# Performance work log

Hardware: AMD Instinct MI355X
Metric: run time of the kernel (lower is better)

The kernel has to match this reference:

```python
import jax, jax.numpy as jnp
import numpy as np

B, N, D, E, MULT = 4, 512, 1024, 8, 4
H = D * MULT
CAPACITY_FACTOR = 1.0
EPSILON = 1e-6


def setup_inputs() -> dict:
    key = jax.random.key(0)
    ks = jax.random.split(key, 4)
    s1 = 1.0 / np.sqrt(D)
    s2 = 1.0 / np.sqrt(H)
    return {
        "x": jax.random.normal(ks[0], (B, N, D), jnp.float32),
        "w_gate": jax.random.uniform(ks[1], (D, E), jnp.float32, -s1, s1),
        "b_gate": jnp.zeros((E,), jnp.float32),
        "w1": jax.random.uniform(ks[2], (E, D, H), jnp.float32, -s1, s1),
        "b1": jnp.zeros((E, H), jnp.float32),
        "w2": jax.random.uniform(ks[3], (E, H, D), jnp.float32, -s2, s2),
        "b2": jnp.zeros((E, D), jnp.float32),
    }


def _cv_squared(v):
    # torch: x.float().var() is unbiased (ddof=1)
    eps = 1e-10
    m = jnp.mean(v)
    return jnp.var(v, ddof=1) / (m * m + eps)


def reference(x, w_gate, b_gate, w1, b1, w2, b2):
    b, n, d = x.shape
    e = w_gate.shape[1]
    capacity = float(int(CAPACITY_FACTOR * b))  # int(capacity_factor * x.size(0))

    # SwitchGate
    gate = jax.nn.softmax(x @ w_gate + b_gate, axis=-1)          # [B,N,E]
    top_idx = jnp.argmax(gate, axis=-1)                          # [B,N]  == topk(1) indices
    # faithful to torch scatter_(dim=1, top_k_indices, 1): mask[bi, idx[bi,ni,0], 0] = 1
    mask = jnp.zeros_like(gate).at[jnp.arange(b)[:, None], top_idx, 0].set(1.0)
    masked = gate * mask
    denom = masked.sum(0, keepdims=True) + EPSILON               # [1,N,E]
    gate_scores = masked / denom * capacity                      # [B,N,E]
    importance = gate_scores.sum(0)                              # [N,E]
    load = (gate_scores > 0).sum(0).astype(jnp.float32)          # [N,E]
    loss = _cv_squared(importance) + _cv_squared(load)

    # Experts: FeedForward(dim, dim, mult) = Linear -> GELU(exact) -> Linear, all E at once
    h = jax.nn.gelu(jnp.einsum('bnd,edh->bneh', x, w1) + b1, approximate=False)  # [B,N,E,H]
    expert_out = jnp.einsum('bneh,ehd->bned', h, w2) + b2                        # [B,N,E,D]

    # moe_output = sum(gate_scores.unsqueeze(-2) * stacked_expert_outputs, dim=-1)
    out = jnp.einsum('bne,bned->bnd', gate_scores, expert_out)                   # [B,N,D]
    return out, loss
```

## Files before the change

kernel.cpp:

```cpp
#include <hip/hip_runtime.h>
#include <math.h>

static constexpr int Bb = 4;
static constexpr int Nn = 512;
static constexpr int Dd = 1024;
static constexpr int Ee = 8;
static constexpr int Hh = 4096;
static constexpr float CAP = 4.0f;
static constexpr float EPS = 1e-6f;

static constexpr int P1S = 32;
static constexpr int P2S = 64;

__global__ __launch_bounds__(256) void k_gate(
    const float* __restrict__ x, const float* __restrict__ wg,
    const float* __restrict__ bg, int* __restrict__ smask,
    float* __restrict__ gate0, float* __restrict__ xT)
{
    __shared__ float swg[Ee * 1028];
    const int tid = threadIdx.x;
    for (int i = tid; i < Dd * Ee; i += 256) {
        int d = i >> 3, e = i & 7;
        swg[e * 1028 + d] = wg[i];
    }
    __syncthreads();
    const int lane = tid & 63;
    const int tok = blockIdx.x * 4 + (tid >> 6);
    const float* xr = x + (size_t)tok * Dd;
    float acc[Ee];
#pragma unroll
    for (int e = 0; e < Ee; ++e) acc[e] = 0.f;
#pragma unroll
    for (int j = 0; j < 4; ++j) {
        const int d0 = j * 256 + lane * 4;
        float4 xv = *(const float4*)(xr + d0);
#pragma unroll
        for (int e = 0; e < Ee; ++e) {
            float4 wv = *(const float4*)(&swg[e * 1028 + d0]);
            acc[e] = fmaf(xv.x, wv.x, acc[e]);
            acc[e] = fmaf(xv.y, wv.y, acc[e]);
            acc[e] = fmaf(xv.z, wv.z, acc[e]);
            acc[e] = fmaf(xv.w, wv.w, acc[e]);
        }
    }
#pragma unroll
    for (int e = 0; e < Ee; ++e) {
        float v = acc[e];
#pragma unroll
        for (int off = 32; off > 0; off >>= 1) v += __shfl_xor(v, off, 64);
        acc[e] = v + bg[e];
    }
    const int n = tok & (Nn - 1);
    const int b = tok >> 9;
    if (n < 8) {
        const int t32 = b * 8 + n;
        for (int d = lane; d < Dd; d += 64) xT[d * 32 + t32] = xr[d];
    }
    if (lane == 0) {
        int best = 0;
        float bv = acc[0];
#pragma unroll
        for (int e = 1; e < Ee; ++e)
            if (acc[e] > bv) { bv = acc[e]; best = e; }
        atomicOr(&smask[b], 1 << best);
        if (n < 8) {
            float m = acc[0];
#pragma unroll
            for (int e = 1; e < Ee; ++e) m = fmaxf(m, acc[e]);
            float s = 0.f;
#pragma unroll
            for (int e = 0; e < Ee; ++e) s += expf(acc[e] - m);
            gate0[b * 8 + n] = expf(acc[0] - m) / s;
        }
    }
}

__global__ __launch_bounds__(64) void k_score(
    const int* __restrict__ smask, const float* __restrict__ gate0,
    float* __restrict__ gs, float* __restrict__ loss_out)
{
    if (threadIdx.x == 0) {
        float imp[8], ld[8], gsl[32];
        for (int n = 0; n < 8; ++n) {
            float mv[4];
            float den = 0.f;
            for (int b = 0; b < 4; ++b) {
                float g = ((smask[b] >> n) & 1) ? gate0[b * 8 + n] : 0.f;
                mv[b] = g;
                den += g;
            }
            den += EPS;
            float s = 0.f, cnt = 0.f;
            for (int b = 0; b < 4; ++b) {
                float v = mv[b] / den * CAP;
                gsl[b * 8 + n] = v;
                s += v;
                if (v > 0.f) cnt += 1.f;
            }
            imp[n] = s;
            ld[n] = cnt;
        }
        for (int i = 0; i < 32; ++i) gs[i] = gsl[i];
        const float M = (float)(Nn * Ee);
        float si = 0.f, sl = 0.f;
        for (int n = 0; n < 8; ++n) { si += imp[n]; sl += ld[n]; }
        const float mi = si / M, ml = sl / M;
        float di = 0.f, dl = 0.f;
        for (int n = 0; n < 8; ++n) {
            di += (imp[n] - mi) * (imp[n] - mi);
            dl += (ld[n] - ml) * (ld[n] - ml);
        }
        di += (M - 8.f) * mi * mi;
        dl += (M - 8.f) * ml * ml;
        const float vi = di / (M - 1.f), vl = dl / (M - 1.f);
        *loss_out = vi / (mi * mi + 1e-10f) + vl / (ml * ml + 1e-10f);
    }
}

__global__ __launch_bounds__(256) void k_ffn1(
    const float* __restrict__ w1, const float* __restrict__ xT,
    float* __restrict__ p1)
{
    __shared__ float xs[32 * 32];
    const int tid = threadIdx.x;
    {
        float4 v = *(const float4*)(xT + blockIdx.y * (32 * 32) + tid * 4);
        *(float4*)(xs + tid * 4) = v;
    }
    __syncthreads();
    const int h = blockIdx.x * 512 + tid * 2;
    const int k0 = blockIdx.y * 32;
    const float* wp = w1 + (size_t)k0 * Hh + h;
    float2 acc[32];
#pragma unroll
    for (int t = 0; t < 32; ++t) acc[t] = make_float2(0.f, 0.f);
#pragma unroll
    for (int half = 0; half < 2; ++half) {
        float2 wbuf[16];
#pragma unroll
        for (int kk = 0; kk < 16; ++kk)
            wbuf[kk] = *(const float2*)(wp + (size_t)(half * 16 + kk) * Hh);
#pragma unroll
        for (int kk = 0; kk < 16; ++kk) {
            const float4* xrow = (const float4*)(xs + (half * 16 + kk) * 32);
            const float2 w = wbuf[kk];
#pragma unroll
            for (int t4 = 0; t4 < 8; ++t4) {
                float4 xv = xrow[t4];
                acc[t4 * 4 + 0].x = fmaf(xv.x, w.x, acc[t4 * 4 + 0].x);
                acc[t4 * 4 + 0].y = fmaf(xv.x, w.y, acc[t4 * 4 + 0].y);
                acc[t4 * 4 + 1].x = fmaf(xv.y, w.x, acc[t4 * 4 + 1].x);
                acc[t4 * 4 + 1].y = fmaf(xv.y, w.y, acc[t4 * 4 + 1].y);
                acc[t4 * 4 + 2].x = fmaf(xv.z, w.x, acc[t4 * 4 + 2].x);
                acc[t4 * 4 + 2].y = fmaf(xv.z, w.y, acc[t4 * 4 + 2].y);
                acc[t4 * 4 + 3].x = fmaf(xv.w, w.x, acc[t4 * 4 + 3].x);
                acc[t4 * 4 + 3].y = fmaf(xv.w, w.y, acc[t4 * 4 + 3].y);
            }
        }
    }
    float* o = p1 + ((size_t)blockIdx.y * 32) * Hh + h;
#pragma unroll
    for (int t = 0; t < 32; ++t) { *(float2*)o = acc[t]; o += Hh; }
}

__global__ __launch_bounds__(256) void k_h(
    const float* __restrict__ p1, const float* __restrict__ b1,
    float* __restrict__ hT)
{
    const int idx = blockIdx.x * 256 + threadIdx.x;
    const int hh = idx & (Hh - 1);
    const int t = idx >> 12;
    float s = b1[hh];
#pragma unroll
    for (int q = 0; q < P1S; ++q)
        s += p1[((size_t)(q * 32 + t)) * Hh + hh];
    hT[(size_t)hh * 32 + t] = 0.5f * s * (1.f + erff(s * 0.70710678118654752440f));
}

__global__ __launch_bounds__(256) void k_ffn2(
    const float* __restrict__ w2, const float* __restrict__ hT,
    float* __restrict__ p2)
{
    __shared__ float hs[64 * 32];
    const int tid = threadIdx.x;
    {
        float4 v0 = *(const float4*)(hT + blockIdx.y * (64 * 32) + tid * 8);
        float4 v1 = *(const float4*)(hT + blockIdx.y * (64 * 32) + tid * 8 + 4);
        *(float4*)(hs + tid * 8) = v0;
        *(float4*)(hs + tid * 8 + 4) = v1;
    }
    __syncthreads();
    const int d = blockIdx.x * 256 + tid;
    const int k0 = blockIdx.y * 64;
    const float* wp = w2 + (size_t)k0 * Dd + d;
    float acc[32];
#pragma unroll
    for (int t = 0; t < 32; ++t) acc[t] = 0.f;
#pragma unroll
    for (int q = 0; q < 4; ++q) {
        float wbuf[16];
#pragma unroll
        for (int kk = 0; kk < 16; ++kk)
            wbuf[kk] = wp[(size_t)(q * 16 + kk) * Dd];
#pragma unroll
        for (int kk = 0; kk < 16; ++kk) {
            const float4* xrow = (const float4*)(hs + (q * 16 + kk) * 32);
            const float w = wbuf[kk];
#pragma unroll
            for (int t4 = 0; t4 < 8; ++t4) {
                float4 xv = xrow[t4];
                acc[t4 * 4 + 0] = fmaf(xv.x, w, acc[t4 * 4 + 0]);
                acc[t4 * 4 + 1] = fmaf(xv.y, w, acc[t4 * 4 + 1]);
                acc[t4 * 4 + 2] = fmaf(xv.z, w, acc[t4 * 4 + 2]);
                acc[t4 * 4 + 3] = fmaf(xv.w, w, acc[t4 * 4 + 3]);
            }
        }
    }
    float* o = p2 + ((size_t)blockIdx.y * 32) * Dd + d;
#pragma unroll
    for (int t = 0; t < 32; ++t) { *o = acc[t]; o += Dd; }
}

__global__ __launch_bounds__(256) void k_out(
    const float* __restrict__ p2, const float* __restrict__ b2,
    const float* __restrict__ gs, float* __restrict__ out)
{
    const int row = blockIdx.x;
    const int d4 = threadIdx.x * 4;
    const int n = row & (Nn - 1);
    float4 o = make_float4(0.f, 0.f, 0.f, 0.f);
    if (n < 8) {
        const int b = row >> 9;
        const int t = b * 8 + n;
        const float g = gs[t];
        float4 a = make_float4(0.f, 0.f, 0.f, 0.f);
        const float* p = p2 + (size_t)t * Dd + d4;
#pragma unroll 8
        for (int s = 0; s < P2S; ++s) {
            float4 v = *(const float4*)p;
            p += (size_t)32 * Dd;
            a.x += v.x; a.y += v.y; a.z += v.z; a.w += v.w;
        }
        float4 bb = *(const float4*)(b2 + d4);
        o.x = g * (a.x + bb.x);
        o.y = g * (a.y + bb.y);
        o.z = g * (a.z + bb.z);
        o.w = g * (a.w + bb.w);
    }
    *(float4*)(out + (size_t)row * Dd + d4) = o;
}

extern "C" void kernel_launch(void* const* d_in, const int* in_sizes, int n_in,
                              void* d_out, int out_size, void* d_ws, size_t ws_size,
                              hipStream_t stream) {
    const float* x  = (const float*)d_in[0];
    const float* wg = (const float*)d_in[1];
    const float* bg = (const float*)d_in[2];
    const float* w1 = (const float*)d_in[3];
    const float* b1 = (const float*)d_in[4];
    const float* w2 = (const float*)d_in[5];
    const float* b2 = (const float*)d_in[6];
    float* out = (float*)d_out;

    float* wsf   = (float*)d_ws;
    int*   smask = (int*)d_ws;
    float* gate0 = wsf + 64;
    float* gs    = wsf + 128;
    float* xT    = wsf + 256;
    float* hT    = wsf + 36864;
    float* p1    = wsf + 167936;
    float* p2    = wsf + 4362240;

    hipMemsetAsync(smask, 0, 4 * sizeof(int), stream);
    k_gate<<<dim3(Bb * Nn / 4), dim3(256), 0, stream>>>(x, wg, bg, smask, gate0, xT);
    k_score<<<dim3(1), dim3(64), 0, stream>>>(smask, gate0, gs, out + (out_size - 1));
    k_ffn1<<<dim3(8, P1S), dim3(256), 0, stream>>>(w1, xT, p1);
    k_h<<<dim3(512), dim3(256), 0, stream>>>(p1, b1, hT);
    k_ffn2<<<dim3(4, P2S), dim3(256), 0, stream>>>(w2, hT, p2);
    k_out<<<dim3(Bb * Nn), dim3(256), 0, stream>>>(p2, b2, gs, out);
}
```

Before: 299.9 us.

## Fuse gate, FFN1 and output zeroing into one launch; merge GELU with scoring

Folds the gate projection, the first FFN partial-product GEMM and the zero-fill of unused output rows into a single kernel using block-index ranges, and reads x directly instead of staging a transposed copy. The GELU reduction and the loss/score computation share one launch, with the scoring done by one wave using shuffles instead of a serial thread. The per-batch atomic mask and the memset are replaced by per-block masks, and FFN2 is retiled to fewer, deeper K splits with 128-thread blocks. This cuts launch count and redundant memory traffic, but the output pass now writes only active rows, so it relies on the fused zeroing to cover the rest.

```diff
diff --git a/kernel.cpp b/kernel.cpp
--- a/kernel.cpp
+++ b/kernel.cpp
@@ -10,201 +10,243 @@
 static constexpr float EPS = 1e-6f;
 
 static constexpr int P1S = 32;
-static constexpr int P2S = 64;
-
-__global__ __launch_bounds__(256) void k_gate(
+static constexpr int P2S = 32;
+
+
+__global__ __launch_bounds__(256) void k1_gate_ffn1(
     const float* __restrict__ x, const float* __restrict__ wg,
-    const float* __restrict__ bg, int* __restrict__ smask,
-    float* __restrict__ gate0, float* __restrict__ xT)
+    const float* __restrict__ bg, const float* __restrict__ w1,
+    int* __restrict__ bmask, float* __restrict__ gate0,
+    float* __restrict__ p1, float* __restrict__ out)
 {
-    __shared__ float swg[Ee * 1028];
+    __shared__ float smem[8 * 1028 + 16];
+    const int blk = blockIdx.x;
     const int tid = threadIdx.x;
-    for (int i = tid; i < Dd * Ee; i += 256) {
-        int d = i >> 3, e = i & 7;
-        swg[e * 1028 + d] = wg[i];
-    }
-    __syncthreads();
-    const int lane = tid & 63;
-    const int tok = blockIdx.x * 4 + (tid >> 6);
-    const float* xr = x + (size_t)tok * Dd;
-    float acc[Ee];
-#pragma unroll
-    for (int e = 0; e < Ee; ++e) acc[e] = 0.f;
-#pragma unroll
-    for (int j = 0; j < 4; ++j) {
-        const int d0 = j * 256 + lane * 4;
-        float4 xv = *(const float4*)(xr + d0);
-#pragma unroll
-        for (int e = 0; e < Ee; ++e) {
-            float4 wv = *(const float4*)(&swg[e * 1028 + d0]);
-            acc[e] = fmaf(xv.x, wv.x, acc[e]);
-            acc[e] = fmaf(xv.y, wv.y, acc[e]);
-            acc[e] = fmaf(xv.z, wv.z, acc[e]);
-            acc[e] = fmaf(xv.w, wv.w, acc[e]);
-        }
-    }
-#pragma unroll
-    for (int e = 0; e < Ee; ++e) {
-        float v = acc[e];
-#pragma unroll
-        for (int off = 32; off > 0; off >>= 1) v += __shfl_xor(v, off, 64);
-        acc[e] = v + bg[e];
-    }
-    const int n = tok & (Nn - 1);
-    const int b = tok >> 9;
-    if (n < 8) {
-        const int t32 = b * 8 + n;
-        for (int d = lane; d < Dd; d += 64) xT[d * 32 + t32] = xr[d];
-    }
-    if (lane == 0) {
-        int best = 0;
-        float bv = acc[0];
-#pragma unroll
-        for (int e = 1; e < Ee; ++e)
-            if (acc[e] > bv) { bv = acc[e]; best = e; }
-        atomicOr(&smask[b], 1 << best);
-        if (n < 8) {
-            float m = acc[0];
-#pragma unroll
-            for (int e = 1; e < Ee; ++e) m = fmaxf(m, acc[e]);
-            float s = 0.f;
-#pragma unroll
-            for (int e = 0; e < Ee; ++e) s += expf(acc[e] - m);
-            gate0[b * 8 + n] = expf(acc[0] - m) / s;
-        }
-    }
-}
-
-__global__ __launch_bounds__(64) void k_score(
-    const int* __restrict__ smask, const float* __restrict__ gate0,
-    float* __restrict__ gs, float* __restrict__ loss_out)
+
+    if (blk < 256) {
+        const int hc = blk & 7, ks = blk >> 3, k0 = ks * 32;
+        {
+            const int t = tid >> 3, q = tid & 7;
+            const int row = (t >> 3) * Nn + (t & 7);
+            float4 v = *(const float4*)(x + (size_t)row * Dd + k0 + q * 4);
+            smem[(q * 4 + 0) * 32 + t] = v.x;
+            smem[(q * 4 + 1) * 32 + t] = v.y;
+            smem[(q * 4 + 2) * 32 + t] = v.z;
+            smem[(q * 4 + 3) * 32 + t] = v.w;
+        }
+        __syncthreads();
+        const int h = hc * 512 + tid * 2;
+        const float* wp = w1 + (size_t)k0 * Hh + h;
+        float2 acc[32];
+#pragma unroll
+        for (int t = 0; t < 32; ++t) acc[t] = make_float2(0.f, 0.f);
+#pragma unroll
+        for (int half = 0; half < 2; ++half) {
+            float2 wbuf[16];
+#pragma unroll
+            for (int kk = 0; kk < 16; ++kk)
+                wbuf[kk] = *(const float2*)(wp + (size_t)(half * 16 + kk) * Hh);
+#pragma unroll
+            for (int kk = 0; kk < 16; ++kk) {
+                const float4* xrow = (const float4*)(smem + (half * 16 + kk) * 32);
+                const float2 w = wbuf[kk];
+#pragma unroll
+                for (int t4 = 0; t4 < 8; ++t4) {
+                    float4 xv = xrow[t4];
+                    acc[t4 * 4 + 0].x = fmaf(xv.x, w.x, acc[t4 * 4 + 0].x);
+                    acc[t4 * 4 + 0].y = fmaf(xv.x, w.y, acc[t4 * 4 + 0].y);
+                    acc[t4 * 4 + 1].x = fmaf(xv.y, w.x, acc[t4 * 4 + 1].x);
+                    acc[t4 * 4 + 1].y = fmaf(xv.y, w.y, acc[t4 * 4 + 1].y);
+                    acc[t4 * 4 + 2].x = fmaf(xv.z, w.x, acc[t4 * 4 + 2].x);
+                    acc[t4 * 4 + 2].y = fmaf(xv.z, w.y, acc[t4 * 4 + 2].y);
+                    acc[t4 * 4 + 3].x = fmaf(xv.w, w.x, acc[t4 * 4 + 3].x);
+                    acc[t4 * 4 + 3].y = fmaf(xv.w, w.y, acc[t4 * 4 + 3].y);
+                }
+            }
+        }
+        float* o = p1 + ((size_t)ks * 32) * Hh + h;
+#pragma unroll
+        for (int t = 0; t < 32; ++t) { *(float2*)o = acc[t]; o += Hh; }
+    } else if (blk < 512) {
+        const int g = blk - 256;
+        for (int i = tid; i < Dd * Ee; i += 256)
+            smem[(i & 7) * 1028 + (i >> 3)] = wg[i];
+        int* bb = (int*)&smem[8224];
+        __syncthreads();
+        const int wave = tid >> 6, lane = tid & 63;
+        for (int j = 0; j < 2; ++j) {
+            const int sub = wave + 4 * j;
+            const int tok = g * 8 + sub;
+            const float* xr = x + (size_t)tok * Dd;
+            float acc[Ee];
+#pragma unroll
+            for (int e = 0; e < Ee; ++e) acc[e] = 0.f;
+#pragma unroll
+            for (int jj = 0; jj < 4; ++jj) {
+                const int d0 = jj * 256 + lane * 4;
+                float4 xv = *(const float4*)(xr + d0);
+#pragma unroll
+                for (int e = 0; e < Ee; ++e) {
+                    float4 wv = *(const float4*)(&smem[e * 1028 + d0]);
+                    acc[e] = fmaf(xv.x, wv.x, acc[e]);
+                    acc[e] = fmaf(xv.y, wv.y, acc[e]);
+                    acc[e] = fmaf(xv.z, wv.z, acc[e]);
+                    acc[e] = fmaf(xv.w, wv.w, acc[e]);
+                }
+            }
+#pragma unroll
+            for (int e = 0; e < Ee; ++e) {
+                float v = acc[e];
+#pragma unroll
+                for (int off = 32; off > 0; off >>= 1) v += __shfl_xor(v, off, 64);
+                acc[e] = v + bg[e];
+            }
+            if (lane == 0) {
+                int best = 0;
+                float bv = acc[0];
+#pragma unroll
+                for (int e = 1; e < Ee; ++e)
+                    if (acc[e] > bv) { bv = acc[e]; best = e; }
+                bb[sub] = 1 << best;
+                const int n = tok & (Nn - 1);
+                const int b = tok >> 9;
+                if (n < 8) {
+                    float m = acc[0];
+#pragma unroll
+                    for (int e = 1; e < Ee; ++e) m = fmaxf(m, acc[e]);
+                    float s = 0.f;
+#pragma unroll
+                    for (int e = 0; e < Ee; ++e) s += expf(acc[e] - m);
+                    gate0[b * 8 + n] = expf(acc[0] - m) / s;
+                }
+            }
+        }
+        __syncthreads();
+        if (tid == 0) {
+            int m = 0;
+#pragma unroll
+            for (int i = 0; i < 8; ++i) m |= bb[i];
+            bmask[g] = m;
+        }
+    } else {
+        const int z = blk - 512;
+        const float4 zero4 = make_float4(0.f, 0.f, 0.f, 0.f);
+#pragma unroll
+        for (int r = 0; r < 8; ++r) {
+            const int row = z * 8 + r;
+            const int n = row & (Nn - 1);
+            if (n >= 8)
+                *(float4*)(out + (size_t)row * Dd + tid * 4) = zero4;
+        }
+    }
+}
+
+__global__ __launch_bounds__(128) void k2_gelu_score(
+    const float* __restrict__ p1, const float* __restrict__ b1,
+    float* __restrict__ hT, const int* __restrict__ bmask,
+    const float* __restrict__ gate0, float* __restrict__ gs,
+    float* __restrict__ loss_out)
 {
-    if (threadIdx.x == 0) {
-        float imp[8], ld[8], gsl[32];
-        for (int n = 0; n < 8; ++n) {
-            float mv[4];
-            float den = 0.f;
-            for (int b = 0; b < 4; ++b) {
-                float g = ((smask[b] >> n) & 1) ? gate0[b * 8 + n] : 0.f;
-                mv[b] = g;
-                den += g;
-            }
-            den += EPS;
-            float s = 0.f, cnt = 0.f;
-            for (int b = 0; b < 4; ++b) {
-                float v = mv[b] / den * CAP;
-                gsl[b * 8 + n] = v;
-                s += v;
-                if (v > 0.f) cnt += 1.f;
-            }
-            imp[n] = s;
-            ld[n] = cnt;
-        }
-        for (int i = 0; i < 32; ++i) gs[i] = gsl[i];
+    const int blk = blockIdx.x, tid = threadIdx.x;
+    if (blk < 256) {
+        const int idx = blk * 128 + tid;
+        const int hh0 = (idx << 2) & (Hh - 1);
+        const int t = idx >> 10;
+        float4 s = *(const float4*)(b1 + hh0);
+#pragma unroll
+        for (int q = 0; q < P1S; ++q) {
+            float4 v = *(const float4*)(p1 + ((size_t)(q * 32 + t)) * Hh + hh0);
+            s.x += v.x; s.y += v.y; s.z += v.z; s.w += v.w;
+        }
+        const float c = 0.70710678118654752440f;
+        float4 r;
+        r.x = 0.5f * s.x * (1.f + erff(s.x * c));
+        r.y = 0.5f * s.y * (1.f + erff(s.y * c));
+        r.z = 0.5f * s.z * (1.f + erff(s.z * c));
+        r.w = 0.5f * s.w * (1.f + erff(s.w * c));
+        *(float4*)(hT + (size_t)t * Hh + hh0) = r;
+    } else if (tid < 64) {
+        const int l = tid;
+        int m0 = bmask[l], m1 = bmask[64 + l], m2 = bmask[128 + l], m3 = bmask[192 + l];
+#pragma unroll
+        for (int off = 32; off > 0; off >>= 1) {
+            m0 |= __shfl_xor(m0, off, 64);
+            m1 |= __shfl_xor(m1, off, 64);
+            m2 |= __shfl_xor(m2, off, 64);
+            m3 |= __shfl_xor(m3, off, 64);
+        }
+        float gm = 0.f;
+        if (l < 32) {
+            const int b = l >> 3, n = l & 7;
+            const int sm = (b == 0) ? m0 : (b == 1) ? m1 : (b == 2) ? m2 : m3;
+            if ((sm >> n) & 1) gm = gate0[l];
+        }
+        float den = gm + __shfl_xor(gm, 8, 64);
+        den += __shfl_xor(den, 16, 64);
+        float gsv = 0.f;
+        if (l < 32) { gsv = gm / (den + EPS) * CAP; gs[l] = gsv; }
+        float impn = gsv + __shfl_xor(gsv, 8, 64); impn += __shfl_xor(impn, 16, 64);
+        float ldv = (gsv > 0.f) ? 1.f : 0.f;
+        float ldn = ldv + __shfl_xor(ldv, 8, 64); ldn += __shfl_xor(ldn, 16, 64);
+        float si = gsv, sl = ldv;
+#pragma unroll
+        for (int off = 32; off > 0; off >>= 1) {
+            si += __shfl_xor(si, off, 64);
+            sl += __shfl_xor(sl, off, 64);
+        }
         const float M = (float)(Nn * Ee);
-        float si = 0.f, sl = 0.f;
-        for (int n = 0; n < 8; ++n) { si += imp[n]; sl += ld[n]; }
         const float mi = si / M, ml = sl / M;
-        float di = 0.f, dl = 0.f;
-        for (int n = 0; n < 8; ++n) {
-            di += (imp[n] - mi) * (imp[n] - mi);
-            dl += (ld[n] - ml) * (ld[n] - ml);
-        }
-        di += (M - 8.f) * mi * mi;
-        dl += (M - 8.f) * ml * ml;
-        const float vi = di / (M - 1.f), vl = dl / (M - 1.f);
-        *loss_out = vi / (mi * mi + 1e-10f) + vl / (ml * ml + 1e-10f);
-    }
-}
-
-__global__ __launch_bounds__(256) void k_ffn1(
-    const float* __restrict__ w1, const float* __restrict__ xT,
-    float* __restrict__ p1)
-{
-    __shared__ float xs[32 * 32];
-    const int tid = threadIdx.x;
-    {
-        float4 v = *(const float4*)(xT + blockIdx.y * (32 * 32) + tid * 4);
-        *(float4*)(xs + tid * 4) = v;
-    }
-    __syncthreads();
-    const int h = blockIdx.x * 512 + tid * 2;
-    const int k0 = blockIdx.y * 32;
-    const float* wp = w1 + (size_t)k0 * Hh + h;
-    float2 acc[32];
-#pragma unroll
-    for (int t = 0; t < 32; ++t) acc[t] = make_float2(0.f, 0.f);
-#pragma unroll
-    for (int half = 0; half < 2; ++half) {
-        float2 wbuf[16];
-#pragma unroll
-        for (int kk = 0; kk < 16; ++kk)
-            wbuf[kk] = *(const float2*)(wp + (size_t)(half * 16 + kk) * Hh);
-#pragma unroll
-        for (int kk = 0; kk < 16; ++kk) {
-            const float4* xrow = (const float4*)(xs + (half * 16 + kk) * 32);
-            const float2 w = wbuf[kk];
-#pragma unroll
-            for (int t4 = 0; t4 < 8; ++t4) {
-                float4 xv = xrow[t4];
-                acc[t4 * 4 + 0].x = fmaf(xv.x, w.x, acc[t4 * 4 + 0].x);
-                acc[t4 * 4 + 0].y = fmaf(xv.x, w.y, acc[t4 * 4 + 0].y);
-                acc[t4 * 4 + 1].x = fmaf(xv.y, w.x, acc[t4 * 4 + 1].x);
-                acc[t4 * 4 + 1].y = fmaf(xv.y, w.y, acc[t4 * 4 + 1].y);
-                acc[t4 * 4 + 2].x = fmaf(xv.z, w.x, acc[t4 * 4 + 2].x);
-                acc[t4 * 4 + 2].y = fmaf(xv.z, w.y, acc[t4 * 4 + 2].y);
-                acc[t4 * 4 + 3].x = fmaf(xv.w, w.x, acc[t4 * 4 + 3].x);
-                acc[t4 * 4 + 3].y = fmaf(xv.w, w.y, acc[t4 * 4 + 3].y);
-            }
-        }
-    }
-    float* o = p1 + ((size_t)blockIdx.y * 32) * Hh + h;
-#pragma unroll
-    for (int t = 0; t < 32; ++t) { *(float2*)o = acc[t]; o += Hh; }
-}
-
-__global__ __launch_bounds__(256) void k_h(
-    const float* __restrict__ p1, const float* __restrict__ b1,
-    float* __restrict__ hT)
-{
-    const int idx = blockIdx.x * 256 + threadIdx.x;
-    const int hh = idx & (Hh - 1);
-    const int t = idx >> 12;
-    float s = b1[hh];
-#pragma unroll
-    for (int q = 0; q < P1S; ++q)
-        s += p1[((size_t)(q * 32 + t)) * Hh + hh];
-    hT[(size_t)hh * 32 + t] = 0.5f * s * (1.f + erff(s * 0.70710678118654752440f));
-}
-
-__global__ __launch_bounds__(256) void k_ffn2(
+        float di = (l < 8) ? (impn - mi) * (impn - mi) : 0.f;
+        float dl = (l < 8) ? (ldn - ml) * (ldn - ml) : 0.f;
+#pragma unroll
+        for (int off = 32; off > 0; off >>= 1) {
+            di += __shfl_xor(di, off, 64);
+            dl += __shfl_xor(dl, off, 64);
+        }
+        if (l == 0) {
+            di += (M - 8.f) * mi * mi;
+            dl += (M - 8.f) * ml * ml;
+            const float vi = di / (M - 1.f), vl = dl / (M - 1.f);
+            *loss_out = vi / (mi * mi + 1e-10f) + vl / (ml * ml + 1e-10f);
+        }
+    }
+}
+
+__global__ __launch_bounds__(128) void k3_ffn2(
     const float* __restrict__ w2, const float* __restrict__ hT,
     float* __restrict__ p2)
 {
-    __shared__ float hs[64 * 32];
+    __shared__ float smem[128 * 32];
     const int tid = threadIdx.x;
+    const int ky = blockIdx.y;
     {
-        float4 v0 = *(const float4*)(hT + blockIdx.y * (64 * 32) + tid * 8);
-        float4 v1 = *(const float4*)(hT + blockIdx.y * (64 * 32) + tid * 8 + 4);
-        *(float4*)(hs + tid * 8) = v0;
-        *(float4*)(hs + tid * 8 + 4) = v1;
+        const int t = tid & 31, kq = tid >> 5;
+        const float* src = hT + (size_t)t * Hh + ky * 128 + kq * 32;
+#pragma unroll
+        for (int c = 0; c < 8; ++c) {
+            float4 v = *(const float4*)(src + c * 4);
+            smem[(kq * 32 + c * 4 + 0) * 32 + t] = v.x;
+            smem[(kq * 32 + c * 4 + 1) * 32 + t] = v.y;
+            smem[(kq * 32 + c * 4 + 2) * 32 + t] = v.z;
+            smem[(kq * 32 + c * 4 + 3) * 32 + t] = v.w;
+        }
     }
     __syncthreads();
-    const int d = blockIdx.x * 256 + tid;
-    const int k0 = blockIdx.y * 64;
+    const int d = blockIdx.x * 128 + tid;
+    const int k0 = ky * 128;
     const float* wp = w2 + (size_t)k0 * Dd + d;
     float acc[32];
 #pragma unroll
     for (int t = 0; t < 32; ++t) acc[t] = 0.f;
 #pragma unroll
-    for (int q = 0; q < 4; ++q) {
+    for (int q = 0; q < 8; ++q) {
         float wbuf[16];
 #pragma unroll
         for (int kk = 0; kk < 16; ++kk)
             wbuf[kk] = wp[(size_t)(q * 16 + kk) * Dd];
 #pragma unroll
         for (int kk = 0; kk < 16; ++kk) {
-            const float4* xrow = (const float4*)(hs + (q * 16 + kk) * 32);
+            const float4* xrow = (const float4*)(smem + (q * 16 + kk) * 32);
             const float w = wbuf[kk];
 #pragma unroll
             for (int t4 = 0; t4 < 8; ++t4) {
@@ -216,38 +258,34 @@
             }
         }
     }
-    float* o = p2 + ((size_t)blockIdx.y * 32) * Dd + d;
+    float* o = p2 + ((size_t)ky * 32) * Dd + d;
 #pragma unroll
     for (int t = 0; t < 32; ++t) { *o = acc[t]; o += Dd; }
 }
 
-__global__ __launch_bounds__(256) void k_out(
+__global__ __launch_bounds__(128) void k4_out(
     const float* __restrict__ p2, const float* __restrict__ b2,
     const float* __restrict__ gs, float* __restrict__ out)
 {
-    const int row = blockIdx.x;
-    const int d4 = threadIdx.x * 4;
-    const int n = row & (Nn - 1);
-    float4 o = make_float4(0.f, 0.f, 0.f, 0.f);
-    if (n < 8) {
-        const int b = row >> 9;
-        const int t = b * 8 + n;
-        const float g = gs[t];
-        float4 a = make_float4(0.f, 0.f, 0.f, 0.f);
-        const float* p = p2 + (size_t)t * Dd + d4;
+    const int t = blockIdx.x >> 1;
+    const int d4 = (blockIdx.x & 1) * 512 + threadIdx.x * 4;
+    float4 a = make_float4(0.f, 0.f, 0.f, 0.f);
+    const float* p = p2 + (size_t)t * Dd + d4;
 #pragma unroll 8
-        for (int s = 0; s < P2S; ++s) {
-            float4 v = *(const float4*)p;
-            p += (size_t)32 * Dd;
-            a.x += v.x; a.y += v.y; a.z += v.z; a.w += v.w;
-        }
-        float4 bb = *(const float4*)(b2 + d4);
-        o.x = g * (a.x + bb.x);
-        o.y = g * (a.y + bb.y);
-        o.z = g * (a.z + bb.z);
-        o.w = g * (a.w + bb.w);
-    }
-    *(float4*)(out + (size_t)row * Dd + d4) = o;
+    for (int s = 0; s < P2S; ++s) {
+        float4 v = *(const float4*)p;
+        p += (size_t)32 * Dd;
+        a.x += v.x; a.y += v.y; a.z += v.z; a.w += v.w;
+    }
+    float4 bbv = *(const float4*)(b2 + d4);
+    const float g = gs[t];
+    const int b = t >> 3, n = t & 7;
+    float4 o;
+    o.x = g * (a.x + bbv.x);
+    o.y = g * (a.y + bbv.y);
+    o.z = g * (a.z + bbv.z);
+    o.w = g * (a.w + bbv.w);
+    *(float4*)(out + ((size_t)(b * Nn + n)) * Dd + d4) = o;
 }
 
 extern "C" void kernel_launch(void* const* d_in, const int* in_sizes, int n_in,
@@ -261,21 +299,18 @@
     const float* w2 = (const float*)d_in[5];
     const float* b2 = (const float*)d_in[6];
     float* out = (float*)d_out;
-
-    float* wsf   = (float*)d_ws;
-    int*   smask = (int*)d_ws;
-    float* gate0 = wsf + 64;
-    float* gs    = wsf + 128;
-    float* xT    = wsf + 256;
-    float* hT    = wsf + 36864;
-    float* p1    = wsf + 167936;
-    float* p2    = wsf + 4362240;
-
-    hipMemsetAsync(smask, 0, 4 * sizeof(int), stream);
-    k_gate<<<dim3(Bb * Nn / 4), dim3(256), 0, stream>>>(x, wg, bg, smask, gate0, xT);
-    k_score<<<dim3(1), dim3(64), 0, stream>>>(smask, gate0, gs, out + (out_size - 1));
-    k_ffn1<<<dim3(8, P1S), dim3(256), 0, stream>>>(w1, xT, p1);
-    k_h<<<dim3(512), dim3(256), 0, stream>>>(p1, b1, hT);
-    k_ffn2<<<dim3(4, P2S), dim3(256), 0, stream>>>(w2, hT, p2);
-    k_out<<<dim3(Bb * Nn), dim3(256), 0, stream>>>(p2, b2, gs, out);
-}
+    float* wsf = (float*)d_ws;
+
+    int*   bmask = (int*)d_ws;
+    float* gate0 = wsf + 256;
+    float* gs    = wsf + 320;
+    float* hT    = wsf + 512;
+    float* p1    = wsf + 132096;
+    float* p2    = wsf + 4326400;
+
+    k1_gate_ffn1<<<dim3(768), dim3(256), 0, stream>>>(x, wg, bg, w1, bmask, gate0, p1, out);
+    k2_gelu_score<<<dim3(257), dim3(128), 0, stream>>>(p1, b1, hT, bmask, gate0, gs,
+                                                       out + (out_size - 1));
+    k3_ffn2<<<dim3(8, 32), dim3(128), 0, stream>>>(w2, hT, p2);
+    k4_out<<<dim3(64), dim3(128), 0, stream>>>(p2, b2, gs, out);
+}
```

Result: faster. 266.5 us (-11.1%).
